# Kernel optimization log

Measured on AMD Instinct MI355X. Metric: run time of the kernel, lower is better.

## Reference

```python
import jax, jax.numpy as jnp
import numpy as np
import math

H, KVH, D = 15, 5, 64  # heads, kv heads, head_dim
ROPE_BASE = 10000.0
NEG = -1e9


def _rope_cos_sin(position_ids):
    # position_ids: [B, S] int -> cos/sin [B, 1, S, D]
    inv_freq = 1.0 / (ROPE_BASE ** (jnp.arange(0, D, 2, dtype=jnp.float32) / D))  # [D/2]
    freqs = position_ids.astype(jnp.float32)[..., None] * inv_freq  # [B, S, D/2]
    emb = jnp.concatenate([freqs, freqs], axis=-1)  # [B, S, D]
    return jnp.cos(emb)[:, None], jnp.sin(emb)[:, None]


def _rotate_half(x):
    x1, x2 = x[..., : D // 2], x[..., D // 2 :]
    return jnp.concatenate([-x2, x1], axis=-1)


def setup_inputs() -> dict:
    key = jax.random.key(0)
    ks = jax.random.split(key, 5)
    B, S, E = 1, 4096, 960
    hidden_states = jax.random.normal(ks[0], (B, S, E), dtype=jnp.float32)
    Wq = jax.random.normal(ks[1], (E, E), dtype=jnp.float32) * 0.02
    Wk = jax.random.normal(ks[2], (KVH * D, E), dtype=jnp.float32) * 0.02
    Wv = jax.random.normal(ks[3], (KVH * D, E), dtype=jnp.float32) * 0.02
    Wo = jax.random.normal(ks[4], (E, E), dtype=jnp.float32) * 0.02
    causal = jnp.tril(jnp.ones((S, S), dtype=bool))
    attention_mask = jnp.where(causal, 0.0, NEG).astype(jnp.float32)[None, None]  # [1,1,S,S]
    position_ids = jnp.arange(S, dtype=jnp.int64 if jax.config.jax_enable_x64 else jnp.int32)[None]
    return {
        "hidden_states": hidden_states,
        "Wq": Wq,
        "Wk": Wk,
        "Wv": Wv,
        "Wo": Wo,
        "attention_mask": attention_mask,
        "position_ids": position_ids,
    }


def reference(hidden_states, Wq, Wk, Wv, Wo, attention_mask, position_ids):
    B, S, E = hidden_states.shape
    groups = H // KVH
    # projections (bias-free Linear: x @ W.T)
    q = (hidden_states @ Wq.T).reshape(B, S, H, D).transpose(0, 2, 1, 3)      # [B,H,S,D]
    k = (hidden_states @ Wk.T).reshape(B, S, KVH, D).transpose(0, 2, 1, 3)    # [B,KVH,S,D]
    v = (hidden_states @ Wv.T).reshape(B, S, KVH, D).transpose(0, 2, 1, 3)    # [B,KVH,S,D]
    cos, sin = _rope_cos_sin(position_ids)  # [B,1,S,D]
    q = q * cos + _rotate_half(q) * sin
    k = k * cos + _rotate_half(k) * sin
    # GQA: repeat_interleave over the head axis
    k = jnp.repeat(k, groups, axis=1)  # [B,H,S,D]
    v = jnp.repeat(v, groups, axis=1)  # [B,H,S,D]
    scores = jnp.einsum("bhqd,bhkd->bhqk", q, k) / math.sqrt(D) + attention_mask
    probs = jax.nn.softmax(scores.astype(jnp.float32), axis=-1).astype(q.dtype)
    out = jnp.einsum("bhqk,bhkd->bhqd", probs, v)  # [B,H,S,D]
    out = out.transpose(0, 2, 1, 3).reshape(B, S, E)
    return out @ Wo.T
```

## Files before the change

### kernel.cpp

```cpp
#include <hip/hip_runtime.h>
#include <hip/hip_bf16.h>

typedef __hip_bfloat16 bf16;
typedef short bf16x8 __attribute__((ext_vector_type(8)));
typedef short bf16x4 __attribute__((ext_vector_type(4)));
typedef float f32x4 __attribute__((ext_vector_type(4)));

static constexpr int S_LEN = 4096;
static constexpr int EMB   = 960;
static constexpr int NH    = 15;
static constexpr int NKVH  = 5;
static constexpr int KV_E  = NKVH * 64;

__device__ __forceinline__ float scrub(float x, float lim) {
  return fminf(fmaxf(x, -lim), lim);
}

__device__ __forceinline__ short f2bf(float x) {
  bf16 h = __float2bfloat16(x);
  short s;
  __builtin_memcpy(&s, &h, 2);
  return s;
}

__device__ __forceinline__ void stage16(const bf16* g, bf16* l) {
  __builtin_amdgcn_global_load_lds(
      (const __attribute__((address_space(1))) void*)g,
      (__attribute__((address_space(3))) void*)l, 16, 0, 0);
}

__global__ void cvt5_kernel(const float* s0, const float* s1, const float* s2,
                            const float* s3, const float* s4,
                            bf16* d0, bf16* d1, bf16* d2, bf16* d3, bf16* d4,
                            int e0, int e1, int e2, int e3, int e4) {
  int i = blockIdx.x * blockDim.x + threadIdx.x;
  const float* s;
  bf16* d;
  int base;
  if (i < e0)      { s = s0; d = d0; base = 0;  }
  else if (i < e1) { s = s1; d = d1; base = e0; }
  else if (i < e2) { s = s2; d = d2; base = e1; }
  else if (i < e3) { s = s3; d = d3; base = e2; }
  else if (i < e4) { s = s4; d = d4; base = e3; }
  else return;
  int k = i - base;
  const float4* sp = (const float4*)s + (size_t)k * 2;
  float4 a = sp[0], b = sp[1];
  bf16x8 r;
  r[0] = f2bf(a.x); r[1] = f2bf(a.y); r[2] = f2bf(a.z); r[3] = f2bf(a.w);
  r[4] = f2bf(b.x); r[5] = f2bf(b.y); r[6] = f2bf(b.z); r[7] = f2bf(b.w);
  *(bf16x8*)((short*)d + (size_t)k * 8) = r;
}

template <typename EPI>
__device__ __forceinline__ void gemm_core(
    const bf16* __restrict__ A, const bf16* __restrict__ W,
    int m0, int n0, int K, bf16* At0, bf16* At1, bf16* Bt0, bf16* Bt1,
    EPI&& epilogue) {
  const int lane = threadIdx.x & 63;
  const int wave = threadIdx.x >> 6;
  const int quad = lane >> 4;
  const int c16  = lane & 15;
  const int wm = wave >> 1, wn = wave & 1;
  const int srow = lane >> 2;
  const int sch  = lane & 3;
  const int NIT  = K / 32;
  bf16* At[2] = {At0, At1};
  bf16* Bt[2] = {Bt0, Bt1};

  auto stage = [&](int b, int k0) {
#pragma unroll
    for (int t = 0; t < 2; t++) {
      int j = wave * 2 + t;
      stage16(A + (size_t)(m0 + j * 16 + srow) * K + k0 + sch * 8,
              At[b] + j * 512);
      stage16(W + (size_t)(n0 + j * 16 + srow) * K + k0 + sch * 8,
              Bt[b] + j * 512);
    }
  };

  f32x4 acc[4][4];
#pragma unroll
  for (int i = 0; i < 4; i++)
#pragma unroll
    for (int j = 0; j < 4; j++) acc[i][j] = (f32x4){0.f, 0.f, 0.f, 0.f};

  stage(0, 0);
  __syncthreads();

  for (int it = 0; it < NIT; ++it) {
    if (it + 1 < NIT) stage((it + 1) & 1, (it + 1) * 32);
    const char* ab = (const char*)At[it & 1];
    const char* bb = (const char*)Bt[it & 1];
    bf16x8 af[4], bfr[4];
#pragma unroll
    for (int i = 0; i < 4; i++)
      af[i] = *(const bf16x8*)(ab + (wm * 64 + i * 16 + c16) * 64 + quad * 16);
#pragma unroll
    for (int j = 0; j < 4; j++)
      bfr[j] = *(const bf16x8*)(bb + (wn * 64 + j * 16 + c16) * 64 + quad * 16);
#pragma unroll
    for (int i = 0; i < 4; i++)
#pragma unroll
      for (int j = 0; j < 4; j++)
        acc[i][j] = __builtin_amdgcn_mfma_f32_16x16x32_bf16(af[i], bfr[j],
                                                            acc[i][j], 0, 0, 0);
    __syncthreads();
  }
  epilogue(acc, m0, n0, wm, wn, quad, c16);
}

__global__ __launch_bounds__(256) void gemm_qkv_kernel(
    const bf16* __restrict__ A, const bf16* __restrict__ Wcat,
    bf16* __restrict__ Qb, bf16* __restrict__ Kbf, bf16* __restrict__ VTb,
    int M, int K) {
  __shared__ __align__(16) bf16 At[2][128 * 32];
  __shared__ __align__(16) bf16 Bt[2][128 * 32];
  const int m0 = blockIdx.x * 128;
  const int n0 = blockIdx.y * 128;
  gemm_core(A, Wcat, m0, n0, K, At[0], At[1], Bt[0], Bt[1],
            [&](f32x4 (&acc)[4][4], int m0_, int n0_, int wm, int wn,
                int quad, int c16) {
#pragma unroll
              for (int i = 0; i < 4; i++)
#pragma unroll
                for (int j = 0; j < 4; j++) {
                  int scol = n0_ + wn * 64 + j * 16;
                  if (scol >= 1600) continue;
                  int colg = scol + c16;
                  int row0 = m0_ + wm * 64 + i * 16 + quad * 4;
                  if (scol < 960) {
#pragma unroll
                    for (int r = 0; r < 4; r++)
                      Qb[(size_t)(row0 + r) * EMB + colg] =
                          __float2bfloat16(scrub(acc[i][j][r], 3e4f));
                  } else if (scol < 1280) {
#pragma unroll
                    for (int r = 0; r < 4; r++)
                      Kbf[(size_t)(row0 + r) * KV_E + (colg - 960)] =
                          __float2bfloat16(scrub(acc[i][j][r], 3e4f));
                  } else {
                    bf16x4 v;
#pragma unroll
                    for (int r = 0; r < 4; r++)
                      v[r] = f2bf(scrub(acc[i][j][r], 3e4f));
                    int t0 = m0_ + wm * 64;
                    int nl = quad * 8 + (i >> 1) * 32 + (i & 1) * 4;
                    *(bf16x4*)((short*)VTb + (size_t)(colg - 1280) * S_LEN +
                               t0 + nl) = v;
                  }
                }
            });
}

__global__ __launch_bounds__(256) void gemm_out_kernel(
    const bf16* __restrict__ A, const bf16* __restrict__ W,
    float* __restrict__ C, int M, int N, int K) {
  __shared__ __align__(16) bf16 At[2][128 * 32];
  __shared__ __align__(16) bf16 Bt[2][128 * 32];
  const int m0 = blockIdx.x * 128;
  const int n0 = blockIdx.y * 128;
  gemm_core(A, W, m0, n0, K, At[0], At[1], Bt[0], Bt[1],
            [&](f32x4 (&acc)[4][4], int m0_, int n0_, int wm, int wn,
                int quad, int c16) {
#pragma unroll
              for (int i = 0; i < 4; i++)
#pragma unroll
                for (int j = 0; j < 4; j++) {
                  int scol = n0_ + wn * 64 + j * 16;
                  if (scol >= EMB) continue;
                  int col = scol + c16;
                  int row0 = m0_ + wm * 64 + i * 16 + quad * 4;
#pragma unroll
                  for (int r = 0; r < 4; r++)
                    C[(size_t)(row0 + r) * EMB + col] =
                        scrub(acc[i][j][r], 3e4f);
                }
            });
}

__global__ void rope2_kernel(bf16* __restrict__ Qb, bf16* __restrict__ Kb,
                             const int* __restrict__ pos_ids) {
  int tid = blockIdx.x * blockDim.x + threadIdx.x;
  if (tid >= S_LEN * (NH + NKVH) * 32) return;
  int d  = tid & 31;
  int hh = (tid >> 5) % (NH + NKVH);
  int s  = tid / ((NH + NKVH) * 32);
  bf16* buf;
  size_t idx;
  float scale;
  if (hh < NH) {
    buf = Qb; idx = (size_t)s * EMB + hh * 64 + d;
    scale = 0.18033688011112042f;
  } else {
    buf = Kb; idx = (size_t)s * KV_E + (hh - NH) * 64 + d; scale = 1.0f;
  }
  float x = __bfloat162float(buf[idx]);
  float y = __bfloat162float(buf[idx + 32]);
  float f = (float)pos_ids[s] * expf((float)d * -0.28782313662425572f);
  float sf, cf;
  sincosf(f, &sf, &cf);
  buf[idx]      = __float2bfloat16(scrub((x * cf - y * sf) * scale, 3e4f));
  buf[idx + 32] = __float2bfloat16(scrub((y * cf + x * sf) * scale, 3e4f));
}

__global__ __launch_bounds__(256, 5) void flash_kernel(
    const bf16* Q, const bf16* __restrict__ Kb,
    const bf16* __restrict__ VT, bf16* O) {
  __shared__ __align__(16) bf16 Kt[2][64 * 64];
  __shared__ __align__(16) bf16 Vt[2][64 * 64];

  const int bx = blockIdx.x;
  const int lane = threadIdx.x & 63;
  const int wv   = threadIdx.x >> 6;
  const int quad = lane >> 4;
  const int c16  = lane & 15;
  const int h    = blockIdx.y;
  const int kvh  = h / 3;

  const int rsub = lane >> 3;
  const int gch  = (lane & 7) ^ rsub;
  const int rm   = c16 & 7;
  const int ko0  = (quad ^ rm) * 16;

  bf16x4 ones4;
#pragma unroll
  for (int j = 0; j < 4; j++) ones4[j] = (short)0x3F80;

  auto stage = [&](int b, int it) {
    const int kbase = it * 64;
#pragma unroll
    for (int t = 0; t < 2; t++) {
      int i = wv * 2 + t;
      int r = i * 8 + rsub;
      stage16(Kb + (size_t)(kbase + r) * KV_E + kvh * 64 + gch * 8,
              &Kt[b][i * 512]);
      stage16(VT + (size_t)(kvh * 64 + r) * S_LEN + kbase + gch * 8,
              &Vt[b][i * 512]);
    }
  };

  auto run_strip = [&](int xq) {
    const int qw   = xq * 64 + wv * 16;
    const int qcol = qw + c16;
    const int itend = xq + 1;

    const bf16* qrow = Q + (size_t)qcol * EMB + h * 64 + quad * 8;
    const bf16x8 aq0 = *(const bf16x8*)qrow;
    const bf16x8 aq1 = *(const bf16x8*)(qrow + 32);

    f32x4 o[4];
#pragma unroll
    for (int n = 0; n < 4; n++) o[n] = (f32x4){0.f, 0.f, 0.f, 0.f};
    f32x4 os = (f32x4){0.f, 0.f, 0.f, 0.f};

    stage(0, 0);
    __syncthreads();

    for (int it = 0; it < itend; ++it) {
      if (it + 1 < itend) stage((it + 1) & 1, it + 1);

      const int kbase = it * 64;
      const char* kb = (const char*)&Kt[it & 1][0];
      const char* vb = (const char*)&Vt[it & 1][0];
      const bool masked = (it == xq);

      bf16x4 pp[4];
#pragma unroll
      for (int cc = 0; cc < 4; cc++) {
        int r = cc * 16 + c16;
        bf16x8 b0 = *(const bf16x8*)(kb + r * 128 + ko0);
        bf16x8 b1 = *(const bf16x8*)(kb + r * 128 + (ko0 ^ 64));
        f32x4 s = (f32x4){0.f, 0.f, 0.f, 0.f};
        s = __builtin_amdgcn_mfma_f32_16x16x32_bf16(b0, aq0, s, 0, 0, 0);
        s = __builtin_amdgcn_mfma_f32_16x16x32_bf16(b1, aq1, s, 0, 0, 0);
#pragma unroll
        for (int r4 = 0; r4 < 4; r4++) {
          float p = exp2f(s[r4]);
          if (masked) {
            int kc = kbase + cc * 16 + quad * 4 + r4;
            p = (kc <= qcol) ? p : 0.f;
          }
          pp[cc][r4] = f2bf(p);
        }
      }

#pragma unroll
      for (int cc = 0; cc < 4; cc++)
        os = __builtin_amdgcn_mfma_f32_16x16x16bf16_1k(ones4, pp[cc], os,
                                                       0, 0, 0);

#pragma unroll
      for (int n = 0; n < 4; n++) {
        const char* vrow = vb + (n * 16 + c16) * 128;
        bf16x8 va = *(const bf16x8*)(vrow + ko0);
        bf16x8 vc = *(const bf16x8*)(vrow + (ko0 ^ 64));
        bf16x4 a0 = __builtin_shufflevector(va, va, 0, 1, 2, 3);
        bf16x4 a1 = __builtin_shufflevector(va, va, 4, 5, 6, 7);
        bf16x4 a2 = __builtin_shufflevector(vc, vc, 0, 1, 2, 3);
        bf16x4 a3 = __builtin_shufflevector(vc, vc, 4, 5, 6, 7);
        o[n] = __builtin_amdgcn_mfma_f32_16x16x16bf16_1k(a0, pp[0], o[n],
                                                         0, 0, 0);
        o[n] = __builtin_amdgcn_mfma_f32_16x16x16bf16_1k(a1, pp[1], o[n],
                                                         0, 0, 0);
        o[n] = __builtin_amdgcn_mfma_f32_16x16x16bf16_1k(a2, pp[2], o[n],
                                                         0, 0, 0);
        o[n] = __builtin_amdgcn_mfma_f32_16x16x16bf16_1k(a3, pp[3], o[n],
                                                         0, 0, 0);
      }

      __syncthreads();
    }

    const float inv = 1.0f / fmaxf(os[0], 1e-20f);
#pragma unroll
    for (int n = 0; n < 4; n++) {
      bf16x4 w;
#pragma unroll
      for (int r = 0; r < 4; r++)
        w[r] = f2bf(scrub(o[n][r] * inv, 1e4f));
      *(bf16x4*)((short*)O + (size_t)qcol * EMB + h * 64 + n * 16 +
                 quad * 4) = w;
    }
  };

  run_strip(63 - bx);
  run_strip(bx);
}

extern "C" void kernel_launch(void* const* d_in, const int* in_sizes, int n_in,
                              void* d_out, int out_size, void* d_ws, size_t ws_size,
                              hipStream_t stream) {
  const float* hs = (const float*)d_in[0];
  const float* Wq = (const float*)d_in[1];
  const float* Wk = (const float*)d_in[2];
  const float* Wv = (const float*)d_in[3];
  const float* Wo = (const float*)d_in[4];
  const int* pos = (const int*)d_in[6];
  float* out = (float*)d_out;

  char* wsb = (char*)d_ws;
  size_t regA = ((size_t)S_LEN * EMB + (size_t)S_LEN * NH) * sizeof(float);
  bf16* hsb = (bf16*)wsb;
  bf16* Qb  = (bf16*)(wsb + regA);
  bf16* Kbf = Qb + (size_t)S_LEN * EMB;
  bf16* VTb = Kbf + (size_t)S_LEN * KV_E;
  bf16* Wqb = VTb + (size_t)S_LEN * KV_E;
  bf16* Wkb = Wqb + (size_t)EMB * EMB;
  bf16* Wvb = Wkb + (size_t)KV_E * EMB;
  bf16* Wob = Wqb + (size_t)1664 * EMB;

  {
    int e0 = (S_LEN * EMB) / 8;
    int e1 = e0 + (EMB * EMB) / 8;
    int e2 = e1 + (KV_E * EMB) / 8;
    int e3 = e2 + (KV_E * EMB) / 8;
    int e4 = e3 + (EMB * EMB) / 8;
    cvt5_kernel<<<(e4 + 255) / 256, 256, 0, stream>>>(
        hs, Wq, Wk, Wv, Wo, hsb, Wqb, Wkb, Wvb, Wob, e0, e1, e2, e3, e4);
  }

  gemm_qkv_kernel<<<dim3(S_LEN / 128, 13), 256, 0, stream>>>(
      hsb, Wqb, Qb, Kbf, VTb, S_LEN, EMB);

  {
    int n = S_LEN * (NH + NKVH) * 32;
    rope2_kernel<<<(n + 255) / 256, 256, 0, stream>>>(Qb, Kbf, pos);
  }

  flash_kernel<<<dim3(32, NH), 256, 0, stream>>>(Qb, Kbf, VTb, Qb);

  gemm_out_kernel<<<dim3(S_LEN / 128, 8), 256, 0, stream>>>(
      Qb, Wob, out, S_LEN, EMB, EMB);
}
```

Baseline: 253.9 us.

## Triple-buffer LDS staging with single barrier and vmcnt waits in GEMM and flash

Both the GEMM core and the flash-attention loop move from double to triple-buffered shared memory. Loads are issued two tiles ahead, and each iteration waits on outstanding global loads with explicit s_waitcnt vmcnt plus a single s_barrier, replacing two __syncthreads. The flash kernel also raises wave priority around its MFMA section and uses 32-bit offset arithmetic for addresses. The extra LDS lowers the flash occupancy hint from 5 to 3 blocks per CU. The vmcnt(4) count relies on stage16 issuing exactly one load per call, which is fragile if that changes.

```diff
diff --git a/kernel.cpp b/kernel.cpp
--- a/kernel.cpp
+++ b/kernel.cpp
@@ -55,8 +55,7 @@
 template <typename EPI>
 __device__ __forceinline__ void gemm_core(
     const bf16* __restrict__ A, const bf16* __restrict__ W,
-    int m0, int n0, int K, bf16* At0, bf16* At1, bf16* Bt0, bf16* Bt1,
-    EPI&& epilogue) {
+    int m0, int n0, int K, bf16* At, bf16* Bt, EPI&& epilogue) {
   const int lane = threadIdx.x & 63;
   const int wave = threadIdx.x >> 6;
   const int quad = lane >> 4;
@@ -65,17 +64,15 @@
   const int srow = lane >> 2;
   const int sch  = lane & 3;
   const int NIT  = K / 32;
-  bf16* At[2] = {At0, At1};
-  bf16* Bt[2] = {Bt0, Bt1};
 
   auto stage = [&](int b, int k0) {
 #pragma unroll
     for (int t = 0; t < 2; t++) {
       int j = wave * 2 + t;
-      stage16(A + (size_t)(m0 + j * 16 + srow) * K + k0 + sch * 8,
-              At[b] + j * 512);
-      stage16(W + (size_t)(n0 + j * 16 + srow) * K + k0 + sch * 8,
-              Bt[b] + j * 512);
+      stage16(A + (unsigned)((m0 + j * 16 + srow) * K + k0 + sch * 8),
+              At + b * 4096 + j * 512);
+      stage16(W + (unsigned)((n0 + j * 16 + srow) * K + k0 + sch * 8),
+              Bt + b * 4096 + j * 512);
     }
   };
 
@@ -86,12 +83,23 @@
     for (int j = 0; j < 4; j++) acc[i][j] = (f32x4){0.f, 0.f, 0.f, 0.f};
 
   stage(0, 0);
-  __syncthreads();
+  stage(1, 32);
+  int ib = 0;
 
   for (int it = 0; it < NIT; ++it) {
-    if (it + 1 < NIT) stage((it + 1) & 1, (it + 1) * 32);
-    const char* ab = (const char*)At[it & 1];
-    const char* bb = (const char*)Bt[it & 1];
+    if (it + 1 < NIT) {
+      asm volatile("s_waitcnt vmcnt(4)" ::: "memory");
+    } else {
+      asm volatile("s_waitcnt vmcnt(0)" ::: "memory");
+    }
+    __builtin_amdgcn_s_barrier();
+    __builtin_amdgcn_sched_barrier(0);
+    if (it + 2 < NIT) {
+      int sb = ib + 2; if (sb >= 3) sb -= 3;
+      stage(sb, (it + 2) * 32);
+    }
+    const char* ab = (const char*)(At + ib * 4096);
+    const char* bb = (const char*)(Bt + ib * 4096);
     bf16x8 af[4], bfr[4];
 #pragma unroll
     for (int i = 0; i < 4; i++)
@@ -105,7 +113,7 @@
       for (int j = 0; j < 4; j++)
         acc[i][j] = __builtin_amdgcn_mfma_f32_16x16x32_bf16(af[i], bfr[j],
                                                             acc[i][j], 0, 0, 0);
-    __syncthreads();
+    ib = (ib + 1 == 3) ? 0 : ib + 1;
   }
   epilogue(acc, m0, n0, wm, wn, quad, c16);
 }
@@ -114,11 +122,11 @@
     const bf16* __restrict__ A, const bf16* __restrict__ Wcat,
     bf16* __restrict__ Qb, bf16* __restrict__ Kbf, bf16* __restrict__ VTb,
     int M, int K) {
-  __shared__ __align__(16) bf16 At[2][128 * 32];
-  __shared__ __align__(16) bf16 Bt[2][128 * 32];
+  __shared__ __align__(16) bf16 At[3][128 * 32];
+  __shared__ __align__(16) bf16 Bt[3][128 * 32];
   const int m0 = blockIdx.x * 128;
   const int n0 = blockIdx.y * 128;
-  gemm_core(A, Wcat, m0, n0, K, At[0], At[1], Bt[0], Bt[1],
+  gemm_core(A, Wcat, m0, n0, K, At[0], Bt[0],
             [&](f32x4 (&acc)[4][4], int m0_, int n0_, int wm, int wn,
                 int quad, int c16) {
 #pragma unroll
@@ -156,11 +164,11 @@
 __global__ __launch_bounds__(256) void gemm_out_kernel(
     const bf16* __restrict__ A, const bf16* __restrict__ W,
     float* __restrict__ C, int M, int N, int K) {
-  __shared__ __align__(16) bf16 At[2][128 * 32];
-  __shared__ __align__(16) bf16 Bt[2][128 * 32];
+  __shared__ __align__(16) bf16 At[3][128 * 32];
+  __shared__ __align__(16) bf16 Bt[3][128 * 32];
   const int m0 = blockIdx.x * 128;
   const int n0 = blockIdx.y * 128;
-  gemm_core(A, W, m0, n0, K, At[0], At[1], Bt[0], Bt[1],
+  gemm_core(A, W, m0, n0, K, At[0], Bt[0],
             [&](f32x4 (&acc)[4][4], int m0_, int n0_, int wm, int wn,
                 int quad, int c16) {
 #pragma unroll
@@ -204,11 +212,11 @@
   buf[idx + 32] = __float2bfloat16(scrub((y * cf + x * sf) * scale, 3e4f));
 }
 
-__global__ __launch_bounds__(256, 5) void flash_kernel(
+__global__ __launch_bounds__(256, 3) void flash_kernel(
     const bf16* Q, const bf16* __restrict__ Kb,
     const bf16* __restrict__ VT, bf16* O) {
-  __shared__ __align__(16) bf16 Kt[2][64 * 64];
-  __shared__ __align__(16) bf16 Vt[2][64 * 64];
+  __shared__ __align__(16) bf16 Kt[3][64 * 64];
+  __shared__ __align__(16) bf16 Vt[3][64 * 64];
 
   const int bx = blockIdx.x;
   const int lane = threadIdx.x & 63;
@@ -233,9 +241,9 @@
     for (int t = 0; t < 2; t++) {
       int i = wv * 2 + t;
       int r = i * 8 + rsub;
-      stage16(Kb + (size_t)(kbase + r) * KV_E + kvh * 64 + gch * 8,
+      stage16(Kb + (unsigned)((kbase + r) * KV_E + kvh * 64 + gch * 8),
               &Kt[b][i * 512]);
-      stage16(VT + (size_t)(kvh * 64 + r) * S_LEN + kbase + gch * 8,
+      stage16(VT + (unsigned)((kvh * 64 + r) * S_LEN + kbase + gch * 8),
               &Vt[b][i * 512]);
     }
   };
@@ -245,6 +253,8 @@
     const int qcol = qw + c16;
     const int itend = xq + 1;
 
+    __syncthreads();
+
     const bf16* qrow = Q + (size_t)qcol * EMB + h * 64 + quad * 8;
     const bf16x8 aq0 = *(const bf16x8*)qrow;
     const bf16x8 aq1 = *(const bf16x8*)(qrow + 32);
@@ -255,17 +265,29 @@
     f32x4 os = (f32x4){0.f, 0.f, 0.f, 0.f};
 
     stage(0, 0);
-    __syncthreads();
+    if (itend > 1) stage(1, 1);
+    int ib = 0;
 
     for (int it = 0; it < itend; ++it) {
-      if (it + 1 < itend) stage((it + 1) & 1, it + 1);
+      if (it + 1 < itend) {
+        asm volatile("s_waitcnt vmcnt(4)" ::: "memory");
+      } else {
+        asm volatile("s_waitcnt vmcnt(0)" ::: "memory");
+      }
+      __builtin_amdgcn_s_barrier();
+      __builtin_amdgcn_sched_barrier(0);
+      if (it + 2 < itend) {
+        int sb = ib + 2; if (sb >= 3) sb -= 3;
+        stage(sb, it + 2);
+      }
 
       const int kbase = it * 64;
-      const char* kb = (const char*)&Kt[it & 1][0];
-      const char* vb = (const char*)&Vt[it & 1][0];
+      const char* kb = (const char*)&Kt[0][0] + ib * 8192;
+      const char* vb = (const char*)&Vt[0][0] + ib * 8192;
       const bool masked = (it == xq);
 
       bf16x4 pp[4];
+      __builtin_amdgcn_s_setprio(1);
 #pragma unroll
       for (int cc = 0; cc < 4; cc++) {
         int r = cc * 16 + c16;
@@ -308,8 +330,9 @@
         o[n] = __builtin_amdgcn_mfma_f32_16x16x16bf16_1k(a3, pp[3], o[n],
                                                          0, 0, 0);
       }
-
-      __syncthreads();
+      __builtin_amdgcn_s_setprio(0);
+
+      ib = (ib + 1 == 3) ? 0 : ib + 1;
     }
 
     const float inv = 1.0f / fmaxf(os[0], 1e-20f);
```

New measurement: 250.7 us. Within noise of the previous version (-1.3%).
